# Performance work log

Hardware: AMD Instinct MI355X
Metric: run time of the kernel (lower is better)

The kernel has to match this reference:

```python
import math
import jax, jax.numpy as jnp
import numpy as np

# ---- matryoshka config (matches init_kwargs) ----
NUM_HEADS = 16
KV_GROUPS = 4
KV_REPEATS = NUM_HEADS // KV_GROUPS
QK_SIZES = [32, 64, 128]      # output_sizes // num_heads
HEAD_SIZES = [32, 64, 128]
D_MODEL = 2048
NEG_INF = -1e9


def _heads_reorder_indices(num_heads, sizes, reverse=False):
    parts = [[] for _ in range(num_heads)]
    offset, prev = 0, 0
    for size in sizes:
        seg = size - prev
        for h in range(num_heads):
            parts[h].append(np.arange(offset, offset + seg))
            offset += seg
        prev = size
    reorder = np.concatenate([a for head in parts for a in head])
    if reverse:
        rev = np.empty_like(reorder)
        rev[reorder] = np.arange(len(reorder))
        reorder = rev
    return jnp.asarray(reorder, dtype=jnp.int32)

Q_REORDER = _heads_reorder_indices(NUM_HEADS, QK_SIZES)
K_REORDER = _heads_reorder_indices(KV_GROUPS, QK_SIZES)
V_REORDER = _heads_reorder_indices(KV_GROUPS, HEAD_SIZES)
O_REORDER = _heads_reorder_indices(NUM_HEADS, HEAD_SIZES, reverse=True)


def setup_inputs() -> dict:
    key = jax.random.key(0)
    ks = jax.random.split(key, 9)
    B, S = 2, 1024
    dq = NUM_HEADS * QK_SIZES[-1]      # 2048
    dkv_q = KV_GROUPS * QK_SIZES[-1]   # 512
    dkv_v = KV_GROUPS * HEAD_SIZES[-1] # 512
    dout = NUM_HEADS * HEAD_SIZES[-1]  # 2048
    s = 0.02
    return {
        "x": jax.random.normal(ks[0], (B, S, D_MODEL), jnp.float32),
        "mask": jnp.tril(jnp.ones((S, S), jnp.bool_)),
        "Wq": jax.random.normal(ks[1], (D_MODEL, dq), jnp.float32) * s,
        "bq": jnp.zeros((dq,), jnp.float32),
        "Wk": jax.random.normal(ks[2], (D_MODEL, dkv_q), jnp.float32) * s,
        "bk": jnp.zeros((dkv_q,), jnp.float32),
        "Wv": jax.random.normal(ks[3], (D_MODEL, dkv_v), jnp.float32) * s,
        "bv": jnp.zeros((dkv_v,), jnp.float32),
        "Wo": jax.random.normal(ks[4], (dout, D_MODEL), jnp.float32) * s,
        "bo": jnp.zeros((D_MODEL,), jnp.float32),
    }


def reference(x, mask, Wq, bq, Wk, bk, Wv, bv, Wo, bo):
    B, S, _ = x.shape
    H, G, R = NUM_HEADS, KV_GROUPS, KV_REPEATS
    Dq, Dh = QK_SIZES[-1], HEAD_SIZES[-1]

    # matryoshka projections (full-size forward) + buffer-indexed reorder
    q = (x @ Wq + bq)[..., Q_REORDER]
    k = (x @ Wk + bk)[..., K_REORDER]
    v = (x @ Wv + bv)[..., V_REORDER]

    q = q.reshape(B, S, H, Dq).transpose(0, 2, 1, 3)   # [B,H,S,Dq]
    k = k.reshape(B, S, G, Dq).transpose(0, 2, 1, 3)   # [B,G,S,Dq]
    v = v.reshape(B, S, G, Dh).transpose(0, 2, 1, 3)   # [B,G,S,Dh]

    # GQA expansion: each group repeated kv_repeats times consecutively
    k = jnp.repeat(k, R, axis=1)  # [B,H,S,Dq]
    v = jnp.repeat(v, R, axis=1)  # [B,H,S,Dh]

    add_mask = jnp.where(mask, 0.0, NEG_INF).astype(x.dtype)  # [S,S]

    xs = []
    dp_cum = 0.0
    prev_qk, prev_hd = 0, 0
    for qk, hd in zip(QK_SIZES, HEAD_SIZES):
        # dot product over the NEW qk segment, accumulated over prefixes
        dp = jnp.einsum('bhqd,bhkd->bhqk', q[..., prev_qk:qk], k[..., prev_qk:qk])
        dp_cum = dp_cum + dp
        logits = dp_cum * (1.0 / math.sqrt(qk)) + add_mask
        attn = jax.nn.softmax(logits, axis=-1)
        # output only the NEW value segment for this nesting level
        xs.append(jnp.einsum('bhqk,bhkd->bhqd', attn, v[..., prev_hd:hd]))
        prev_qk, prev_hd = qk, hd

    out = jnp.concatenate(xs, axis=-1)                 # [B,H,S,Dh]
    out = out.transpose(0, 2, 1, 3).reshape(B, S, H * Dh)
    out = out[..., O_REORDER]
    return out @ Wo + bo
```

## Files before the change

kernel.cpp:

```cpp
#include <hip/hip_runtime.h>

typedef __attribute__((ext_vector_type(8))) __bf16 bf16x8;
typedef __attribute__((ext_vector_type(8))) unsigned short u16x8;
typedef __attribute__((ext_vector_type(4))) float f32x4;

#define XBOFF 0
#define WQKVOFF (XBOFF + 2048 * 2048)
#define WOOFF   (WQKVOFF + 3072 * 2048)
#define QOFF    (WOOFF + 2048 * 2048)
#define KOFF    (QOFF + 2048 * 2048)
#define VTOFF   (KOFF + 2048 * 512)
#define AOFF    (VTOFF + 2048 * 512)
__device__ __align__(16) ushort g_scratch[AOFF + 2048 * 2048];

__device__ __forceinline__ int nest_map(int n, int H) {
    int h = n >> 7, j = n & 127;
    if (j < 32) return h * 32 + j;
    if (j < 64) return H * 32 + h * 32 + (j - 32);
    return H * 64 + h * 64 + (j - 64);
}

__device__ __forceinline__ ushort f2bf(float f) {
    unsigned u = __builtin_bit_cast(unsigned, f);
    u += 0x7fffu + ((u >> 16) & 1u);
    return (ushort)(u >> 16);
}
__device__ __forceinline__ bf16x8 ld_frag(const ushort* p) {
    return __builtin_bit_cast(bf16x8, *(const u16x8*)p);
}
__device__ __forceinline__ float exp2_fast(float x) {
    return __builtin_amdgcn_exp2f(x);
}
__device__ __forceinline__ void glds16(const ushort* g, ushort* s) {
    __builtin_amdgcn_global_load_lds(
        (const __attribute__((address_space(1))) void*)g,
        (__attribute__((address_space(3))) void*)s, 16, 0, 0);
}

__global__ __launch_bounds__(256) void prep_kernel(
    const float* __restrict__ x,
    const float* __restrict__ Wq, const float* __restrict__ Wk,
    const float* __restrict__ Wv, const float* __restrict__ Wo)
{
    const int bx = blockIdx.x;
    const int tid = threadIdx.x;

    if (bx < 2048) {
        size_t i = ((size_t)bx * 256 + tid) * 8;
        float4 f0 = *(const float4*)&x[i];
        float4 f1 = *(const float4*)&x[i + 4];
        union { uint4 v; ushort u[8]; } a;
        a.u[0] = f2bf(f0.x); a.u[1] = f2bf(f0.y); a.u[2] = f2bf(f0.z); a.u[3] = f2bf(f0.w);
        a.u[4] = f2bf(f1.x); a.u[5] = f2bf(f1.y); a.u[6] = f2bf(f1.z); a.u[7] = f2bf(f1.w);
        *(uint4*)&g_scratch[XBOFF + i] = a.v;
        return;
    }

    const float* W; int rowlen, H, mode, dstoff, t;
    if (bx < 3072)      { W = Wq; rowlen = 2048; H = 16; mode = 0; dstoff = WQKVOFF;               t = bx - 2048; }
    else if (bx < 3328) { W = Wk; rowlen = 512;  H = 4;  mode = 0; dstoff = WQKVOFF + 2048 * 2048; t = bx - 3072; }
    else if (bx < 3584) { W = Wv; rowlen = 512;  H = 4;  mode = 0; dstoff = WQKVOFF + 2560 * 2048; t = bx - 3328; }
    else                { W = Wo; rowlen = 2048; H = 16; mode = 1; dstoff = WOOFF;                 t = bx - 3584; }
    const int k0 = (t & 31) * 64;
    const int n0 = (t >> 5) * 64;

    __shared__ ushort T[64][66];
    const int r = tid >> 3, oct = tid & 7;

    #pragma unroll
    for (int rep = 0; rep < 2; ++rep) {
        int rr = r + rep * 32;
        int wrow = mode ? nest_map(k0 + rr, 16) : (k0 + rr);
        int wcol = mode ? (n0 + oct * 8) : nest_map(n0 + oct * 8, H);
        float4 f0 = *(const float4*)&W[(size_t)wrow * rowlen + wcol];
        float4 f1 = *(const float4*)&W[(size_t)wrow * rowlen + wcol + 4];
        ushort* d = &T[rr][oct * 8];
        d[0] = f2bf(f0.x); d[1] = f2bf(f0.y); d[2] = f2bf(f0.z); d[3] = f2bf(f0.w);
        d[4] = f2bf(f1.x); d[5] = f2bf(f1.y); d[6] = f2bf(f1.z); d[7] = f2bf(f1.w);
    }
    __syncthreads();
    #pragma unroll
    for (int rep = 0; rep < 2; ++rep) {
        int rr = r + rep * 32;
        union { uint4 v; ushort u[8]; } cv;
        #pragma unroll
        for (int i = 0; i < 8; ++i) cv.u[i] = T[oct * 8 + i][rr];
        *(uint4*)&g_scratch[dstoff + (size_t)(n0 + rr) * 2048 + k0 + oct * 8] = cv.v;
    }
}

__global__ __launch_bounds__(256) void gemm128_kernel(
    const float* __restrict__ b0, const float* __restrict__ b1,
    const float* __restrict__ b2, float* __restrict__ oext, int mode)
{
    __shared__ __align__(16) ushort SH[2 * 16384];

    const int gx = gridDim.x;
    const int gy = gridDim.y;
    const int id = blockIdx.x + gx * blockIdx.y;
    const int xcd = id & 7, idl = id >> 3;
    const int CM = gy >> 1, CN = gx >> 2;
    const int m_idx = (xcd >> 2) * CM + (idl % CM);
    const int n_idx = (xcd & 3) * CN + (idl / CM);
    const int n0 = n_idx * 128;
    const int m0 = m_idx * 128;

    const int tid = threadIdx.x;
    const int lane = tid & 63, wid = tid >> 6;
    const int wm = wid & 1, wn = wid >> 1;
    const int quad = lane >> 4, l16 = lane & 15;

    const ushort* A  = g_scratch + (mode ? AOFF : XBOFF);
    const ushort* Bt = g_scratch + (mode ? WOOFF : WQKVOFF);

    const bool vpath = (mode == 0) && (n0 >= 2560);
    const float* bias; ushort* outS = nullptr; int c0, oldim, H;
    if (mode == 1)      { bias = b0; c0 = n0; oldim = 2048; H = 0; }
    else if (n0 < 2048) { bias = b0; outS = g_scratch + QOFF; c0 = n0;        oldim = 2048; H = 16; }
    else if (n0 < 2560) { bias = b1; outS = g_scratch + KOFF; c0 = n0 - 2048; oldim = 512;  H = 4; }
    else                { bias = b2; outS = nullptr;          c0 = n0 - 2560; oldim = 512;  H = 4; }

    const int lrow = lane >> 3;
    const int lchunk = (lane & 7) ^ (lrow & 7);

    f32x4 acc[4][4];
    #pragma unroll
    for (int a = 0; a < 4; ++a)
        #pragma unroll
        for (int c = 0; c < 4; ++c) acc[a][c] = f32x4{0.f, 0.f, 0.f, 0.f};

    auto STAGE = [&](int buf, int kt) {
        const int k0 = kt * 64;
        ushort* as_ = SH + buf * 16384;
        ushort* bs_ = as_ + 8192;
        #pragma unroll
        for (int it = 0; it < 4; ++it) {
            int rb = it * 32 + wid * 8;
            int r  = rb + lrow;
            glds16(&A[(size_t)(m0 + r) * 2048 + k0 + lchunk * 8], &as_[rb * 64]);
        }
        #pragma unroll
        for (int it = 0; it < 4; ++it) {
            int rb = it * 32 + wid * 8;
            int r  = rb + lrow;
            glds16(&Bt[(size_t)(n0 + r) * 2048 + k0 + lchunk * 8], &bs_[rb * 64]);
        }
    };

    STAGE(0, 0);
    STAGE(1, 1);

    for (int kt = 0; kt < 32; ++kt) {
        if (kt < 31) asm volatile("s_waitcnt vmcnt(8)" ::: "memory");
        else         asm volatile("s_waitcnt vmcnt(0)" ::: "memory");
        __builtin_amdgcn_s_barrier();

        const ushort* as_ = SH + (kt & 1) * 16384;
        const ushort* bs_ = as_ + 8192;
        #pragma unroll
        for (int kc = 0; kc < 2; ++kc) {
            bf16x8 af[4], bf[4];
            #pragma unroll
            for (int s = 0; s < 4; ++s) {
                int ra = wm * 64 + s * 16 + l16;
                int rbv = wn * 64 + s * 16 + l16;
                int ch = kc * 4 + quad;
                af[s] = ld_frag(&as_[ra * 64 + ((ch ^ (ra & 7)) * 8)]);
                bf[s] = ld_frag(&bs_[rbv * 64 + ((ch ^ (rbv & 7)) * 8)]);
            }
            #pragma unroll
            for (int sm = 0; sm < 4; ++sm)
                #pragma unroll
                for (int sn = 0; sn < 4; ++sn)
                    acc[sm][sn] = __builtin_amdgcn_mfma_f32_16x16x32_bf16(
                        af[sm], bf[sn], acc[sm][sn], 0, 0, 0);
        }
        __builtin_amdgcn_s_barrier();
        if (kt <= 29) STAGE(kt & 1, kt + 2);
    }
    __syncthreads();

    if (vpath) {
        #pragma unroll
        for (int sm = 0; sm < 4; ++sm)
        #pragma unroll
        for (int sn = 0; sn < 4; ++sn)
        #pragma unroll
        for (int i = 0; i < 4; ++i) {
            int r = wm * 64 + sm * 16 + quad * 4 + i;
            int loc = wn * 64 + sn * 16 + l16;
            float v = acc[sm][sn][i] + bias[nest_map(c0 + loc, 4)];
            SH[loc * 128 + (r ^ ((loc & 7) << 3))] = f2bf(v);
        }
        __syncthreads();
        const int dloc = tid >> 1, half = tid & 1;
        const int gg = c0 >> 7, bb = m0 >> 10, sb = m0 & 1023;
        ushort* vt = g_scratch + VTOFF;
        #pragma unroll
        for (int j = 0; j < 8; ++j) {
            int r = half * 64 + j * 8;
            uint4 v = *(uint4*)&SH[dloc * 128 + (r ^ ((dloc & 7) << 3))];
            *(uint4*)&vt[((size_t)((bb * 4 + gg) * 128 + dloc)) * 1024 + sb + r] = v;
        }
    } else {
        #pragma unroll
        for (int sm = 0; sm < 4; ++sm)
        #pragma unroll
        for (int sn = 0; sn < 4; ++sn)
        #pragma unroll
        for (int i = 0; i < 4; ++i) {
            int row = m0 + wm * 64 + sm * 16 + quad * 4 + i;
            int loc = wn * 64 + sn * 16 + l16;
            float v = acc[sm][sn][i];
            if (mode == 1) {
                oext[(size_t)row * 2048 + c0 + loc] = v + bias[c0 + loc];
            } else {
                v += bias[nest_map(c0 + loc, H)];
                outS[(size_t)row * oldim + c0 + loc] = f2bf(v);
            }
        }
    }
}

__global__ __launch_bounds__(256) void attn_kernel()
{
    const ushort* qb = g_scratch + QOFF;
    const ushort* kb = g_scratch + KOFF;
    const ushort* vt = g_scratch + VTOFF;
    ushort* att = g_scratch + AOFF;

    __shared__ __align__(16) ushort Ks[64 * 128];
    __shared__ __align__(16) ushort Vt[128 * 64];
    __shared__ __align__(16) ushort Ps[64 * 64];

    const int x = blockIdx.x, h = blockIdx.y, b = blockIdx.z;
    const int ks_half = x >> 1;
    const int qt = ((x ^ b) & 1) ? ks_half : 15 - ks_half;
    const int g = h >> 2;
    const int q0 = qt * 64;
    const int tid = threadIdx.x;
    const int lane = tid & 63, w = tid >> 6;
    const int quad = lane >> 4, l16 = lane & 15;

    const float sc0 = 0.25503639f;
    const float sc1 = 0.18033688f;
    const float sc2 = 0.12751820f;

    bf16x8 qa[4];
    {
        const ushort* qrow =
            qb + ((size_t)((b * 1024 + q0 + w * 16 + l16) * 16 + h)) * 128;
        #pragma unroll
        for (int kc = 0; kc < 4; ++kc)
            qa[kc] = ld_frag(qrow + kc * 32 + quad * 8);
    }

    float m_s[3][4], l_s[3][4];
    #pragma unroll
    for (int l = 0; l < 3; ++l)
        #pragma unroll
        for (int i = 0; i < 4; ++i) { m_s[l][i] = -1e9f; l_s[l][i] = 0.0f; }
    f32x4 oacc[8];
    #pragma unroll
    for (int t2 = 0; t2 < 8; ++t2) oacc[t2] = f32x4{0.f, 0.f, 0.f, 0.f};
    const f32x4 fz = {0.f, 0.f, 0.f, 0.f};
    const bf16x8 ones = __builtin_bit_cast(bf16x8, u16x8{
        0x3F80, 0x3F80, 0x3F80, 0x3F80, 0x3F80, 0x3F80, 0x3F80, 0x3F80});

    for (int kt = 0; kt <= qt; ++kt) {
        const int k0 = kt * 64;
        {
            int r16 = tid >> 4, oct16 = tid & 15;
            #pragma unroll
            for (int rep = 0; rep < 4; ++rep) {
                int row = r16 + rep * 16;
                *(uint4*)&Ks[row * 128 + ((oct16 ^ (row & 7)) * 8)] =
                    *(const uint4*)&kb[(size_t)((b * 1024 + k0 + row) * 4 + g) * 128 + oct16 * 8];
            }
            int oct = tid & 7, dr = tid >> 3;
            #pragma unroll
            for (int rep = 0; rep < 4; ++rep) {
                int d = dr + rep * 32;
                *(uint4*)&Vt[d * 64 + ((oct ^ (d & 7)) * 8)] =
                    *(const uint4*)&vt[((size_t)((b * 4 + g) * 128 + d)) * 1024 + k0 + oct * 8];
            }
        }
        __syncthreads();

        const bool diag = (kt == qt);

        f32x4 s0[4], s1[4], s2[4];
        __builtin_amdgcn_s_setprio(1);
        #pragma unroll
        for (int n = 0; n < 4; ++n) {
            int r = n * 16 + l16;
            s0[n] = __builtin_amdgcn_mfma_f32_16x16x32_bf16(
                qa[0], ld_frag(&Ks[r * 128 + (((0 + quad) ^ (r & 7)) * 8)]), fz, 0, 0, 0);
        }
        #pragma unroll
        for (int n = 0; n < 4; ++n) {
            int r = n * 16 + l16;
            s1[n] = __builtin_amdgcn_mfma_f32_16x16x32_bf16(
                qa[1], ld_frag(&Ks[r * 128 + (((4 + quad) ^ (r & 7)) * 8)]), s0[n], 0, 0, 0);
        }
        #pragma unroll
        for (int n = 0; n < 4; ++n) {
            int r = n * 16 + l16;
            s2[n] = __builtin_amdgcn_mfma_f32_16x16x32_bf16(
                qa[2], ld_frag(&Ks[r * 128 + (((8 + quad) ^ (r & 7)) * 8)]), s1[n], 0, 0, 0);
        }
        #pragma unroll
        for (int n = 0; n < 4; ++n) {
            int r = n * 16 + l16;
            s2[n] = __builtin_amdgcn_mfma_f32_16x16x32_bf16(
                qa[3], ld_frag(&Ks[r * 128 + (((12 + quad) ^ (r & 7)) * 8)]), s2[n], 0, 0, 0);
        }
        __builtin_amdgcn_s_setprio(0);

        float sv[3][4][4], mx[3][4];
        #pragma unroll
        for (int l = 0; l < 3; ++l)
            #pragma unroll
            for (int i = 0; i < 4; ++i) mx[l][i] = -1e9f;
        #pragma unroll
        for (int n = 0; n < 4; ++n)
            #pragma unroll
            for (int i = 0; i < 4; ++i) {
                bool msk = diag &&
                    (k0 + n * 16 + l16 > q0 + w * 16 + quad * 4 + i);
                float x0 = msk ? -1e9f : s0[n][i] * sc0;
                float x1 = msk ? -1e9f : s1[n][i] * sc1;
                float x2 = msk ? -1e9f : s2[n][i] * sc2;
                sv[0][n][i] = x0; mx[0][i] = fmaxf(mx[0][i], x0);
                sv[1][n][i] = x1; mx[1][i] = fmaxf(mx[1][i], x1);
                sv[2][n][i] = x2; mx[2][i] = fmaxf(mx[2][i], x2);
            }
        #pragma unroll
        for (int d = 1; d < 16; d <<= 1)
            #pragma unroll
            for (int l = 0; l < 3; ++l)
                #pragma unroll
                for (int i = 0; i < 4; ++i)
                    mx[l][i] = fmaxf(mx[l][i], __shfl_xor(mx[l][i], d, 64));
        float al[3][4];
        #pragma unroll
        for (int l = 0; l < 3; ++l)
            #pragma unroll
            for (int i = 0; i < 4; ++i) {
                float mn = fmaxf(m_s[l][i], mx[l][i]);
                al[l][i] = exp2_fast(m_s[l][i] - mn);
                m_s[l][i] = mn;
            }
        #pragma unroll
        for (int n = 0; n < 4; ++n)
            #pragma unroll
            for (int l = 0; l < 3; ++l)
                #pragma unroll
                for (int i = 0; i < 4; ++i)
                    sv[l][n][i] = exp2_fast(sv[l][n][i] - m_s[l][i]);
        #pragma unroll
        for (int t = 0; t < 8; ++t) {
            int lvl = (t < 2) ? 0 : (t < 4) ? 1 : 2;
            #pragma unroll
            for (int i = 0; i < 4; ++i) oacc[t][i] *= al[lvl][i];
        }

        f32x4 racc[3];
        const int obase[3] = {0, 2, 4}, onts[3] = {2, 2, 4}, voffs[3] = {0, 32, 64};
        #pragma unroll
        for (int l = 0; l < 3; ++l) {
            #pragma unroll
            for (int n = 0; n < 4; ++n)
                #pragma unroll
                for (int i = 0; i < 4; ++i) {
                    int prow = w * 16 + quad * 4 + i;
                    int col = n * 16 + l16;
                    Ps[prow * 64 + ((((col >> 3) ^ (prow & 7)) << 3) | (col & 7))] =
                        f2bf(sv[l][n][i]);
                }
            racc[l] = fz;
            __builtin_amdgcn_s_setprio(1);
            #pragma unroll
            for (int kc = 0; kc < 2; ++kc) {
                int prow = w * 16 + l16;
                bf16x8 pa = ld_frag(&Ps[prow * 64 + (((kc * 4 + quad) ^ (prow & 7)) * 8)]);
                racc[l] = __builtin_amdgcn_mfma_f32_16x16x32_bf16(
                    pa, ones, racc[l], 0, 0, 0);
                #pragma unroll
                for (int t = 0; t < 4; ++t) {
                    if (t < onts[l]) {
                        int vd = voffs[l] + t * 16 + l16;
                        bf16x8 vf = ld_frag(&Vt[vd * 64 + (((kc * 4 + quad) ^ (vd & 7)) * 8)]);
                        oacc[obase[l] + t] = __builtin_amdgcn_mfma_f32_16x16x32_bf16(
                            pa, vf, oacc[obase[l] + t], 0, 0, 0);
                    }
                }
            }
            __builtin_amdgcn_s_setprio(0);
        }
        #pragma unroll
        for (int l = 0; l < 3; ++l)
            #pragma unroll
            for (int i = 0; i < 4; ++i)
                l_s[l][i] = l_s[l][i] * al[l][i] + racc[l][i];
        __syncthreads();
    }

    float inv[3][4];
    #pragma unroll
    for (int l = 0; l < 3; ++l)
        #pragma unroll
        for (int i = 0; i < 4; ++i) {
            float L = l_s[l][i];
            inv[l][i] = (L > 0.f) ? (1.0f / L) : 0.f;
        }
    #pragma unroll
    for (int t = 0; t < 8; ++t) {
        int lvl = (t < 2) ? 0 : (t < 4) ? 1 : 2;
        #pragma unroll
        for (int i = 0; i < 4; ++i) {
            int srow = q0 + w * 16 + quad * 4 + i;
            att[(size_t)((b * 1024 + srow) * 16 + h) * 128 + t * 16 + l16] =
                f2bf(oacc[t][i] * inv[lvl][i]);
        }
    }
}

extern "C" void kernel_launch(void* const* d_in, const int* in_sizes, int n_in,
                              void* d_out, int out_size, void* d_ws, size_t ws_size,
                              hipStream_t stream)
{
    const float* x  = (const float*)d_in[0];
    const float* Wq = (const float*)d_in[2];
    const float* bq = (const float*)d_in[3];
    const float* Wk = (const float*)d_in[4];
    const float* bk = (const float*)d_in[5];
    const float* Wv = (const float*)d_in[6];
    const float* bv = (const float*)d_in[7];
    const float* Wo = (const float*)d_in[8];
    const float* bo = (const float*)d_in[9];
    float* out = (float*)d_out;
    (void)d_ws; (void)ws_size;

    dim3 blk(256, 1, 1);
    hipLaunchKernelGGL(prep_kernel, dim3(4608), blk, 0, stream, x, Wq, Wk, Wv, Wo);
    hipLaunchKernelGGL(gemm128_kernel, dim3(24, 16), blk, 0, stream,
                       bq, bk, bv, (float*)nullptr, 0);
    hipLaunchKernelGGL(attn_kernel, dim3(16, 16, 2), blk, 0, stream);
    hipLaunchKernelGGL(gemm128_kernel, dim3(16, 16), blk, 0, stream,
                       bo, nullptr, nullptr, out, 1);
}
```

Baseline: 258.2 us.

## Split attention key range across two blocks and merge partial softmax results

Each query tile's causal key loop is split into two halves handled by separate blocks, which doubles the attention grid. The unnormalized fp32 partial outputs and per-level running max and sum are written to global scratch. A new merge kernel rescales and combines the two halves, normalizes, and writes the bf16 attention output. This is meant to raise parallelism and balance the causal workload, at the cost of extra global traffic for the fp32 partials and one more kernel launch.

```diff
diff --git a/kernel.cpp b/kernel.cpp
--- a/kernel.cpp
+++ b/kernel.cpp
@@ -11,7 +11,9 @@
 #define KOFF    (QOFF + 2048 * 2048)
 #define VTOFF   (KOFF + 2048 * 512)
 #define AOFF    (VTOFF + 2048 * 512)
-__device__ __align__(16) ushort g_scratch[AOFF + 2048 * 2048];
+#define POOFF   (AOFF + 2048 * 2048)
+#define PMLOFF  (POOFF + 2 * 32768 * 128 * 2)
+__device__ __align__(16) ushort g_scratch[PMLOFF + 2 * 32768 * 6 * 2];
 
 __device__ __forceinline__ int nest_map(int n, int H) {
     int h = n >> 7, j = n & 127;
@@ -227,15 +229,18 @@
     const ushort* qb = g_scratch + QOFF;
     const ushort* kb = g_scratch + KOFF;
     const ushort* vt = g_scratch + VTOFF;
-    ushort* att = g_scratch + AOFF;
+    float* PO  = (float*)(g_scratch + POOFF);
+    float* PML = (float*)(g_scratch + PMLOFF);
 
     __shared__ __align__(16) ushort Ks[64 * 128];
     __shared__ __align__(16) ushort Vt[128 * 64];
     __shared__ __align__(16) ushort Ps[64 * 64];
 
     const int x = blockIdx.x, h = blockIdx.y, b = blockIdx.z;
-    const int ks_half = x >> 1;
-    const int qt = ((x ^ b) & 1) ? ks_half : 15 - ks_half;
+    const int qt_idx = x >> 1, c = x & 1;
+    const int qt = (h & 8) ? qt_idx : (15 - qt_idx);
+    const int nk = qt + 1, half = nk >> 1;
+    const int lo = c ? half : 0, hi = c ? nk : half;
     const int g = h >> 2;
     const int q0 = qt * 64;
     const int tid = threadIdx.x;
@@ -267,7 +272,7 @@
     const bf16x8 ones = __builtin_bit_cast(bf16x8, u16x8{
         0x3F80, 0x3F80, 0x3F80, 0x3F80, 0x3F80, 0x3F80, 0x3F80, 0x3F80});
 
-    for (int kt = 0; kt <= qt; ++kt) {
+    for (int kt = lo; kt < hi; ++kt) {
         const int k0 = kt * 64;
         {
             int r16 = tid >> 4, oct16 = tid & 15;
@@ -406,24 +411,68 @@
         __syncthreads();
     }
 
-    float inv[3][4];
-    #pragma unroll
-    for (int l = 0; l < 3; ++l)
-        #pragma unroll
-        for (int i = 0; i < 4; ++i) {
-            float L = l_s[l][i];
-            inv[l][i] = (L > 0.f) ? (1.0f / L) : 0.f;
-        }
+    const size_t rowbase = ((size_t)(c * 2 + b) * 16 + h) * 1024;
     #pragma unroll
     for (int t = 0; t < 8; ++t) {
-        int lvl = (t < 2) ? 0 : (t < 4) ? 1 : 2;
         #pragma unroll
         for (int i = 0; i < 4; ++i) {
             int srow = q0 + w * 16 + quad * 4 + i;
-            att[(size_t)((b * 1024 + srow) * 16 + h) * 128 + t * 16 + l16] =
-                f2bf(oacc[t][i] * inv[lvl][i]);
-        }
-    }
+            PO[(rowbase + srow) * 128 + t * 16 + l16] = oacc[t][i];
+        }
+    }
+    #pragma unroll
+    for (int lvl = 0; lvl < 3; ++lvl) {
+        if ((l16 >> 1) == lvl && l16 < 6) {
+            bool isl = (l16 & 1);
+            #pragma unroll
+            for (int i = 0; i < 4; ++i) {
+                int srow = q0 + w * 16 + quad * 4 + i;
+                PML[(rowbase + srow) * 6 + l16] = isl ? l_s[lvl][i] : m_s[lvl][i];
+            }
+        }
+    }
+}
+
+__global__ __launch_bounds__(256) void merge_kernel()
+{
+    const float* PO  = (const float*)(g_scratch + POOFF);
+    const float* PML = (const float*)(g_scratch + PMLOFF);
+    ushort* att = g_scratch + AOFF;
+
+    const int idx = blockIdx.x * 256 + threadIdx.x;
+    const int R = idx >> 4;
+    const int seg = idx & 15;
+    const int lvl = (seg < 4) ? 0 : (seg < 8) ? 1 : 2;
+    const int NR = 32768;
+
+    float m0 = PML[(size_t)(0 * NR + R) * 6 + 2 * lvl];
+    float l0 = PML[(size_t)(0 * NR + R) * 6 + 2 * lvl + 1];
+    float m1 = PML[(size_t)(1 * NR + R) * 6 + 2 * lvl];
+    float l1 = PML[(size_t)(1 * NR + R) * 6 + 2 * lvl + 1];
+    float M = fmaxf(m0, m1);
+    float w0 = exp2_fast(m0 - M), w1 = exp2_fast(m1 - M);
+    float den = w0 * l0 + w1 * l1;
+    float inv = (den > 0.f) ? (1.0f / den) : 0.f;
+    w0 *= inv; w1 *= inv;
+
+    const int d0 = seg * 8;
+    float4 a0 = *(const float4*)&PO[((size_t)(0 * NR + R)) * 128 + d0];
+    float4 a1 = *(const float4*)&PO[((size_t)(0 * NR + R)) * 128 + d0 + 4];
+    float4 c0 = *(const float4*)&PO[((size_t)(1 * NR + R)) * 128 + d0];
+    float4 c1 = *(const float4*)&PO[((size_t)(1 * NR + R)) * 128 + d0 + 4];
+
+    union { uint4 v; ushort u[8]; } o;
+    o.u[0] = f2bf(w0 * a0.x + w1 * c0.x);
+    o.u[1] = f2bf(w0 * a0.y + w1 * c0.y);
+    o.u[2] = f2bf(w0 * a0.z + w1 * c0.z);
+    o.u[3] = f2bf(w0 * a0.w + w1 * c0.w);
+    o.u[4] = f2bf(w0 * a1.x + w1 * c1.x);
+    o.u[5] = f2bf(w0 * a1.y + w1 * c1.y);
+    o.u[6] = f2bf(w0 * a1.z + w1 * c1.z);
+    o.u[7] = f2bf(w0 * a1.w + w1 * c1.w);
+
+    const int b = R >> 14, h = (R >> 10) & 15, s = R & 1023;
+    *(uint4*)&att[((size_t)((b * 1024 + s) * 16 + h)) * 128 + d0] = o.v;
 }
 
 extern "C" void kernel_launch(void* const* d_in, const int* in_sizes, int n_in,
@@ -446,7 +495,8 @@
     hipLaunchKernelGGL(prep_kernel, dim3(4608), blk, 0, stream, x, Wq, Wk, Wv, Wo);
     hipLaunchKernelGGL(gemm128_kernel, dim3(24, 16), blk, 0, stream,
                        bq, bk, bv, (float*)nullptr, 0);
-    hipLaunchKernelGGL(attn_kernel, dim3(16, 16, 2), blk, 0, stream);
+    hipLaunchKernelGGL(attn_kernel, dim3(32, 16, 2), blk, 0, stream);
+    hipLaunchKernelGGL(merge_kernel, dim3(2048), blk, 0, stream);
     hipLaunchKernelGGL(gemm128_kernel, dim3(16, 16), blk, 0, stream,
                        bo, nullptr, nullptr, out, 1);
 }
```

Measured after the change: 271.1 us. +5.0%, slower.
